# Kernel optimization log

Measured on AMD Instinct MI355X. Metric: run time of the kernel, lower is better.

The kernel has to match this reference:

```python
import jax, jax.numpy as jnp
import numpy as np

DIM, K, B, H, W = 256, 7, 16, 56, 56
EPS = 1e-5

def _conv(x, w, pad, groups=1):
    return jax.lax.conv_general_dilated(
        x, w, window_strides=(1, 1), padding=[(pad, pad), (pad, pad)],
        dimension_numbers=('NCHW', 'OIHW', 'NCHW'), feature_group_count=groups)

def _bn(x, g, b, m, v):
    scale = g / jnp.sqrt(v + EPS)          # [C]
    bias = b - m * scale
    return x * scale[None, :, None, None] + bias[None, :, None, None]

def _silu(x):
    return x * jax.nn.sigmoid(x)

def setup_inputs() -> dict:
    key = jax.random.key(0)
    ks = jax.random.split(key, 12)
    f = lambda k_, shp, s=0.05: jax.random.normal(k_, shp, jnp.float32) * s
    d = {
        'x':   jax.random.normal(ks[0], (B, DIM, H, W), jnp.float32),
        # RepConv branch: dense 3x3 conv + BN, dense 1x1 conv + BN
        'w3':  f(ks[1], (DIM, DIM, 3, 3)),
        'g1':  1.0 + f(ks[2], (DIM,)), 'b1': f(ks[3], (DIM,)),
        'm1':  f(ks[4], (DIM,)),       'v1': jax.random.uniform(ks[4], (DIM,), jnp.float32) + 0.5,
        'w1':  f(ks[5], (DIM, DIM, 1, 1)),
        'g2':  1.0 + f(ks[6], (DIM,)), 'b2': f(ks[7], (DIM,)),
        'm2':  f(ks[8], (DIM,)),       'v2': jax.random.uniform(ks[8], (DIM,), jnp.float32) + 0.5,
        # depthwise branches
        'dw7': f(ks[9], (DIM, 1, 7, 7)),
        'dwk': f(ks[10], (DIM, 1, K, K)),
        # final BN
        'g3':  1.0 + f(ks[11], (DIM,)), 'b3': f(ks[11], (DIM,)),
        'm3':  f(ks[11], (DIM,)),       'v3': jax.random.uniform(ks[11], (DIM,), jnp.float32) + 0.5,
    }
    return d

def reference(x, w3, g1, b1, m1, v1, w1, g2, b2, m2, v2, dw7, dwk, g3, b3, m3, v3):
    # RepConv (train-mode, bn=False): SiLU(BN(conv3x3(x)) + BN(conv1x1(x)))
    rep = _silu(_bn(_conv(x, w3, 1), g1, b1, m1, v1)
                + _bn(_conv(x, w1, 0), g2, b2, m2, v2))
    # parallel depthwise branches
    y = rep + _conv(x, dw7, 3, groups=DIM) + _conv(x, dwk, K // 2, groups=DIM)
    return _silu(_bn(y, g3, b3, m3, v3))
```

## Files before the change

### kernel.cpp

```cpp
#include <hip/hip_runtime.h>
#include <stdint.h>
#include <stddef.h>

#define DIM 256
#define NB 16
#define HH 56
#define WW 56
#define HWP (HH*WW)
#define PH 62
#define PW 62
#define NPIX (NB*HWP)
#define EPSV 1e-5f

using f32x4  = __attribute__((ext_vector_type(4))) float;
using bf16x8 = __attribute__((ext_vector_type(8))) __bf16;

static __device__ __forceinline__ unsigned short f2bf(float f) {
    union { float f; unsigned u; } v; v.f = f;
    unsigned r = v.u + 0x7FFFu + ((v.u >> 16) & 1u);
    return (unsigned short)(r >> 16);
}
static __device__ __forceinline__ float bf2f(unsigned short u) {
    union { unsigned u; float f; } v; v.u = ((unsigned)u) << 16; return v.f;
}
static __device__ __forceinline__ float silu_f(float z) {
    return z / (1.f + __expf(-z));
}

__global__ void prep_weights(
    const float* __restrict__ w3, const float* __restrict__ g1, const float* __restrict__ b1,
    const float* __restrict__ m1, const float* __restrict__ v1, const float* __restrict__ w1,
    const float* __restrict__ g2, const float* __restrict__ b2, const float* __restrict__ m2,
    const float* __restrict__ v2, const float* __restrict__ dw7, const float* __restrict__ dwk,
    const float* __restrict__ g3, const float* __restrict__ b3, const float* __restrict__ m3,
    const float* __restrict__ v3,
    unsigned short* __restrict__ WkT, float* __restrict__ dwm, float* __restrict__ biasm,
    float* __restrict__ sc3, float* __restrict__ bi3)
{
    int co = blockIdx.x, t = threadIdx.x;
    float s1 = g1[co] * rsqrtf(v1[co] + EPSV);
    float s2 = g2[co] * rsqrtf(v2[co] + EPSV);
    float w1v = w1[co*DIM + t] * s2;
    const float* w3r = w3 + (size_t)(co*DIM + t)*9;
#pragma unroll
    for (int s = 0; s < 9; ++s) {
        float v = w3r[s]*s1 + (s == 4 ? w1v : 0.f);
        WkT[((size_t)s*DIM + co)*DIM + t] = f2bf(v);
    }
    if (t < 49) dwm[co*49 + t] = dw7[co*49 + t] + dwk[co*49 + t];
    if (t == 0) {
        biasm[co] = (b1[co] - m1[co]*s1) + (b2[co] - m2[co]*s2);
        float s3 = g3[co] * rsqrtf(v3[co] + EPSV);
        sc3[co] = s3;
        bi3[co] = b3[co] - m3[co]*s3;
    }
}

__global__ void prep_xpad(const float* __restrict__ x, unsigned short* __restrict__ xpad)
{
    __shared__ float lds[64][57];
    int cc = blockIdx.x;
    int ph = blockIdx.y;
    int b  = blockIdx.z;
    int t  = threadIdx.x;
    int c0 = cc*64;
    char* rowc = (char*)xpad + ((size_t)(b*PH + ph)*PW)*(DIM*2) + c0*2;

    if (ph < 3 || ph >= HH + 3) {
        uint4 z = {0u,0u,0u,0u};
#pragma unroll
        for (int j = 0; j < 2; ++j) {
            int idx = j*256 + t;
            if (idx < 496) {
                int pix = idx >> 3, q = idx & 7;
                *(uint4*)(rowc + (size_t)pix*(DIM*2) + q*16) = z;
            }
        }
        return;
    }
    if (t < 48) {
        int p = t >> 3, q = t & 7;
        int pw = (p < 3) ? p : (PW - 6 + p);
        uint4 z = {0u,0u,0u,0u};
        *(uint4*)(rowc + (size_t)pw*(DIM*2) + q*16) = z;
    }
    int h = ph - 3;
#pragma unroll
    for (int j = 0; j < 14; ++j) {
        int idx = j*256 + t;
        int c = idx / 56, w = idx % 56;
        lds[c][w] = x[((size_t)(b*DIM + c0 + c)*HH + h)*WW + w];
    }
    __syncthreads();
#pragma unroll
    for (int j = 0; j < 7; ++j) {
        int idx = j*256 + t;
        int w = idx >> 5, cp = idx & 31;
        unsigned lo = f2bf(lds[2*cp][w]);
        unsigned hi = f2bf(lds[2*cp+1][w]);
        unsigned val = lo | (hi << 16);
        *(unsigned*)(rowc + (size_t)(w + 3)*(DIM*2) + 4*cp) = val;
    }
}

__global__ void depthwise7(const float* __restrict__ x, const float* __restrict__ dwm,
                           unsigned short* __restrict__ dwout)
{
    __shared__ float plane[PH*PW];
    int c = blockIdx.x, b = blockIdx.y, t = threadIdx.x;
    const float* xp = x + ((size_t)b*DIM + c)*HWP;
    float wr[49];
#pragma unroll
    for (int i = 0; i < 49; ++i) wr[i] = dwm[c*49 + i];
#pragma unroll
    for (int j = 0; j < 16; ++j) {
        int idx = j*256 + t;
        if (idx < PH*PW) {
            int ph = idx / PW, pw = idx % PW;
            int h = ph - 3, w = pw - 3;
            float v = 0.f;
            if ((unsigned)h < HH && (unsigned)w < WW) v = xp[h*WW + w];
            plane[idx] = v;
        }
    }
    __syncthreads();
    unsigned short* op = dwout + ((size_t)b*DIM + c)*HWP;
#pragma unroll
    for (int j = 0; j < 4; ++j) {
        int q = j*256 + t;
        if (q < 784) {
            int h = q / 14, w0 = (q % 14)*4;
            float a0=0.f, a1=0.f, a2=0.f, a3=0.f;
#pragma unroll
            for (int dy = 0; dy < 7; ++dy) {
                float row[10];
#pragma unroll
                for (int i = 0; i < 10; ++i) row[i] = plane[(h+dy)*PW + w0 + i];
#pragma unroll
                for (int dx = 0; dx < 7; ++dx) {
                    float wv = wr[dy*7 + dx];
                    a0 += row[dx]   * wv;
                    a1 += row[dx+1] * wv;
                    a2 += row[dx+2] * wv;
                    a3 += row[dx+3] * wv;
                }
            }
            uint2 pk;
            pk.x = (unsigned)f2bf(a0) | ((unsigned)f2bf(a1) << 16);
            pk.y = (unsigned)f2bf(a2) | ((unsigned)f2bf(a3) << 16);
            *(uint2*)&op[h*WW + w0] = pk;
        }
    }
}

__global__ __launch_bounds__(256, 2)
void main_conv(const unsigned short* __restrict__ xpad, const unsigned short* __restrict__ WkT,
               const unsigned short* __restrict__ dwo, const float* __restrict__ biasm,
               const float* __restrict__ sc3, const float* __restrict__ bi3,
               float* __restrict__ out)
{
    __shared__ __align__(16) char smem[65536];
    int t = threadIdx.x;
    int lane = t & 63, wv = t >> 6;
    int wm = wv >> 1, wn = wv & 1;
    int qm = lane & 15, qg = lane >> 4;

    int swz = (((lane & 7) ^ ((lane >> 3) & 7)) << 4);

    uintptr_t gA[4], gB[4];
#pragma unroll
    for (int r = 0; r < 4; ++r) {
        int pixt = r*32 + wv*8 + (lane >> 3);
        int P = blockIdx.x*128 + pixt;
        int bb = P / HWP, rem = P % HWP;
        int h = rem / WW, w = rem % WW;
        gA[r] = (uintptr_t)xpad + ((size_t)((bb*PH + h + 2)*PW + (w + 2))*DIM)*2 + swz;
        int cog = blockIdx.y*128 + pixt;
        gB[r] = (uintptr_t)WkT + ((size_t)cog*DIM)*2 + swz;
    }

    f32x4 acc[4][4] = {};

    auto stage = [&](int s, int buf) {
        int s9 = s >> 2, ch = s & 3;
        int ky = s9 / 3, kx = s9 - ky*3;
        int offA = (ky*PW + kx)*(DIM*2) + ch*128;
        int offB = s9*(DIM*DIM*2) + ch*128;
        char* base = smem + buf*32768;
#pragma unroll
        for (int r = 0; r < 4; ++r) {
            __builtin_amdgcn_global_load_lds(
                (const __attribute__((address_space(1))) void*)(gA[r] + offA),
                (__attribute__((address_space(3))) void*)(base + (r*32 + wv*8)*128),
                16, 0, 0);
            __builtin_amdgcn_global_load_lds(
                (const __attribute__((address_space(1))) void*)(gB[r] + offB),
                (__attribute__((address_space(3))) void*)(base + 16384 + (r*32 + wv*8)*128),
                16, 0, 0);
        }
    };

    int kxo = (qg << 4) ^ ((lane & 7) << 4);
    auto compute = [&](int buf) {
        const char* pA = smem + buf*32768 + (wm*64 + qm)*128;
        const char* pB = smem + buf*32768 + 16384 + (wn*64 + qm)*128;
#pragma unroll
        for (int kk = 0; kk < 2; ++kk) {
            int ko = kxo ^ (kk << 6);
            bf16x8 a[4], b[4];
#pragma unroll
            for (int i = 0; i < 4; ++i) {
                a[i] = *(const bf16x8*)(pA + i*2048 + ko);
                b[i] = *(const bf16x8*)(pB + i*2048 + ko);
            }
#pragma unroll
            for (int i = 0; i < 4; ++i)
#pragma unroll
                for (int j = 0; j < 4; ++j)
                    acc[i][j] = __builtin_amdgcn_mfma_f32_16x16x32_bf16(a[i], b[j], acc[i][j], 0, 0, 0);
        }
    };

    stage(0, 0);
    __syncthreads();
#pragma unroll 1
    for (int it = 0; it < 18; ++it) {
        stage(2*it + 1, 1);
        compute(0);
        __syncthreads();
        if (it < 17) stage(2*it + 2, 0);
        compute(1);
        __syncthreads();
    }

    float* ep = (float*)smem + wv*1088;
#pragma unroll
    for (int mi = 0; mi < 4; ++mi) {
#pragma unroll
        for (int ni = 0; ni < 4; ++ni)
#pragma unroll
            for (int r = 0; r < 4; ++r)
                ep[(ni*16 + qm)*17 + 4*qg + r] = acc[mi][ni][r];
        __syncthreads();
        int P = blockIdx.x*128 + wm*64 + mi*16 + qm;
        int bb = P / HWP, rem = P % HWP;
        size_t obase = (size_t)bb*DIM*HWP + rem;
#pragma unroll
        for (int j = 0; j < 16; ++j) {
            int col = j*4 + qg;
            int cog = blockIdx.y*128 + wn*64 + col;
            float z = ep[col*17 + qm] + biasm[cog];
            float rep = silu_f(z);
            float y = rep + bf2f(dwo[obase + (size_t)cog*HWP]);
            float yy = y * sc3[cog] + bi3[cog];
            out[obase + (size_t)cog*HWP] = silu_f(yy);
        }
        __syncthreads();
    }
}

extern "C" void kernel_launch(void* const* d_in, const int* in_sizes, int n_in,
                              void* d_out, int out_size, void* d_ws, size_t ws_size,
                              hipStream_t stream)
{
    (void)in_sizes; (void)n_in; (void)out_size; (void)ws_size;
    const float* x   = (const float*)d_in[0];
    const float* w3  = (const float*)d_in[1];
    const float* g1  = (const float*)d_in[2];
    const float* b1  = (const float*)d_in[3];
    const float* m1  = (const float*)d_in[4];
    const float* v1  = (const float*)d_in[5];
    const float* w1  = (const float*)d_in[6];
    const float* g2  = (const float*)d_in[7];
    const float* b2  = (const float*)d_in[8];
    const float* m2  = (const float*)d_in[9];
    const float* v2  = (const float*)d_in[10];
    const float* dw7 = (const float*)d_in[11];
    const float* dwk = (const float*)d_in[12];
    const float* g3  = (const float*)d_in[13];
    const float* b3  = (const float*)d_in[14];
    const float* m3  = (const float*)d_in[15];
    const float* v3  = (const float*)d_in[16];
    float* out = (float*)d_out;

    char* ws = (char*)d_ws;
    unsigned short* xpad = (unsigned short*)(ws);
    unsigned short* WkT  = (unsigned short*)(ws + 31490048);
    unsigned short* dwo  = (unsigned short*)(ws + 32669696);
    float* dwm   = (float*)(ws + 58359808);
    float* biasm = (float*)(ws + 58409984);
    float* sc3   = (float*)(ws + 58411008);
    float* bi3   = (float*)(ws + 58412032);

    prep_weights<<<dim3(DIM), dim3(256), 0, stream>>>(
        w3, g1, b1, m1, v1, w1, g2, b2, m2, v2, dw7, dwk, g3, b3, m3, v3,
        WkT, dwm, biasm, sc3, bi3);
    prep_xpad<<<dim3(4, PH, NB), dim3(256), 0, stream>>>(x, xpad);
    depthwise7<<<dim3(DIM, NB), dim3(256), 0, stream>>>(x, dwm, dwo);
    main_conv<<<dim3(NPIX/128, 2), dim3(256), 0, stream>>>(xpad, WkT, dwo, biasm, sc3, bi3, out);
}
```

Measured before the change: 166.3 us.

## Deepen main conv prefetch pipeline, add MFMA priority, widen depthwise tiles

The main GEMM loop now keeps two stages of async global-to-LDS loads in flight, using explicit vmcnt waits and raw barriers instead of __syncthreads after every half-iteration. MFMA blocks are wrapped in s_setprio to favour the matrix issue. The epilogue drops its per-tile barriers because each wave uses a private LDS region. Separately, the depthwise kernel zero-fills a padded 64-wide plane with vector stores, then reads vectorised rows to produce 8 outputs per thread. This is meant to cut load latency exposure and barrier stalls, at the risk of wrong vmcnt accounting or LDS races.

```diff
diff --git a/kernel.cpp b/kernel.cpp
--- a/kernel.cpp
+++ b/kernel.cpp
@@ -106,49 +106,55 @@
 __global__ void depthwise7(const float* __restrict__ x, const float* __restrict__ dwm,
                            unsigned short* __restrict__ dwout)
 {
-    __shared__ float plane[PH*PW];
+    __shared__ float plane[PH][64];
     int c = blockIdx.x, b = blockIdx.y, t = threadIdx.x;
+#pragma unroll
+    for (int j = 0; j < 4; ++j) {
+        int idx = j*256 + t;
+        if (idx < 992) ((f32x4*)plane)[idx] = (f32x4){0.f,0.f,0.f,0.f};
+    }
+    __syncthreads();
     const float* xp = x + ((size_t)b*DIM + c)*HWP;
+#pragma unroll
+    for (int j = 0; j < 13; ++j) {
+        int idx = j*256 + t;
+        if (idx < HWP) {
+            int h = idx / 56, w = idx % 56;
+            plane[h + 3][w + 3] = xp[idx];
+        }
+    }
     float wr[49];
 #pragma unroll
     for (int i = 0; i < 49; ++i) wr[i] = dwm[c*49 + i];
-#pragma unroll
-    for (int j = 0; j < 16; ++j) {
-        int idx = j*256 + t;
-        if (idx < PH*PW) {
-            int ph = idx / PW, pw = idx % PW;
-            int h = ph - 3, w = pw - 3;
-            float v = 0.f;
-            if ((unsigned)h < HH && (unsigned)w < WW) v = xp[h*WW + w];
-            plane[idx] = v;
-        }
-    }
     __syncthreads();
     unsigned short* op = dwout + ((size_t)b*DIM + c)*HWP;
 #pragma unroll
-    for (int j = 0; j < 4; ++j) {
+    for (int j = 0; j < 2; ++j) {
         int q = j*256 + t;
-        if (q < 784) {
-            int h = q / 14, w0 = (q % 14)*4;
-            float a0=0.f, a1=0.f, a2=0.f, a3=0.f;
+        if (q < 392) {
+            int h = q / 7, w0 = (q % 7)*8;
+            float a[8] = {0.f,0.f,0.f,0.f,0.f,0.f,0.f,0.f};
 #pragma unroll
             for (int dy = 0; dy < 7; ++dy) {
-                float row[10];
-#pragma unroll
-                for (int i = 0; i < 10; ++i) row[i] = plane[(h+dy)*PW + w0 + i];
+                const float* row = &plane[h + dy][w0];
+                union { f32x4 v[4]; float s[16]; } rr;
+                rr.v[0] = *(const f32x4*)(row);
+                rr.v[1] = *(const f32x4*)(row + 4);
+                rr.v[2] = *(const f32x4*)(row + 8);
+                rr.v[3] = *(const f32x4*)(row + 12);
 #pragma unroll
                 for (int dx = 0; dx < 7; ++dx) {
                     float wv = wr[dy*7 + dx];
-                    a0 += row[dx]   * wv;
-                    a1 += row[dx+1] * wv;
-                    a2 += row[dx+2] * wv;
-                    a3 += row[dx+3] * wv;
+#pragma unroll
+                    for (int o = 0; o < 8; ++o) a[o] += rr.s[dx + o] * wv;
                 }
             }
-            uint2 pk;
-            pk.x = (unsigned)f2bf(a0) | ((unsigned)f2bf(a1) << 16);
-            pk.y = (unsigned)f2bf(a2) | ((unsigned)f2bf(a3) << 16);
-            *(uint2*)&op[h*WW + w0] = pk;
+            uint4 pk;
+            pk.x = (unsigned)f2bf(a[0]) | ((unsigned)f2bf(a[1]) << 16);
+            pk.y = (unsigned)f2bf(a[2]) | ((unsigned)f2bf(a[3]) << 16);
+            pk.z = (unsigned)f2bf(a[4]) | ((unsigned)f2bf(a[5]) << 16);
+            pk.w = (unsigned)f2bf(a[6]) | ((unsigned)f2bf(a[7]) << 16);
+            *(uint4*)&op[h*WW + w0] = pk;
         }
     }
 }
@@ -213,35 +219,48 @@
                 a[i] = *(const bf16x8*)(pA + i*2048 + ko);
                 b[i] = *(const bf16x8*)(pB + i*2048 + ko);
             }
+            __builtin_amdgcn_s_setprio(1);
 #pragma unroll
             for (int i = 0; i < 4; ++i)
 #pragma unroll
                 for (int j = 0; j < 4; ++j)
                     acc[i][j] = __builtin_amdgcn_mfma_f32_16x16x32_bf16(a[i], b[j], acc[i][j], 0, 0, 0);
+            __builtin_amdgcn_s_setprio(0);
         }
     };
 
+#define VMW8() asm volatile("s_waitcnt vmcnt(8)" ::: "memory")
+#define VMW0() asm volatile("s_waitcnt vmcnt(0)" ::: "memory")
+#define BARX() { asm volatile("" ::: "memory"); __builtin_amdgcn_s_barrier(); asm volatile("" ::: "memory"); }
+
     stage(0, 0);
-    __syncthreads();
+    stage(1, 1);
+    VMW8(); BARX();
 #pragma unroll 1
-    for (int it = 0; it < 18; ++it) {
-        stage(2*it + 1, 1);
-        compute(0);
-        __syncthreads();
-        if (it < 17) stage(2*it + 2, 0);
-        compute(1);
-        __syncthreads();
-    }
+    for (int s = 0; s < 36; ++s) {
+        compute(s & 1);
+        BARX();
+        if (s <= 33) {
+            stage(s + 2, s & 1);
+            VMW8();
+            BARX();
+        } else if (s == 34) {
+            VMW0();
+            BARX();
+        }
+    }
+#undef VMW8
+#undef VMW0
+#undef BARX
 
     float* ep = (float*)smem + wv*1088;
-#pragma unroll
+#pragma unroll 1
     for (int mi = 0; mi < 4; ++mi) {
 #pragma unroll
         for (int ni = 0; ni < 4; ++ni)
 #pragma unroll
             for (int r = 0; r < 4; ++r)
                 ep[(ni*16 + qm)*17 + 4*qg + r] = acc[mi][ni][r];
-        __syncthreads();
         int P = blockIdx.x*128 + wm*64 + mi*16 + qm;
         int bb = P / HWP, rem = P % HWP;
         size_t obase = (size_t)bb*DIM*HWP + rem;
@@ -255,7 +274,6 @@
             float yy = y * sc3[cog] + bi3[cog];
             out[obase + (size_t)cog*HWP] = silu_f(yy);
         }
-        __syncthreads();
     }
 }
 
```

After: 170.6 us. +2.6%, slower.
